# Kernel tuning notes

Hardware: AMD Instinct MI355X
Metric: run time of the kernel (lower is better)

The kernel has to match this reference:

```python
import jax, jax.numpy as jnp
import numpy as np

N = 50000          # num nodes
E = 600000         # num edges
F_IN = 128         # num_features
H = 128            # graph_hidden_dim
R = 2              # num_relations
L = 3              # n_layers_conv
BN_EPS = 1e-5
BN_BETA = 1e-4     # BatchNorm bias init per module code


def setup_inputs() -> dict:
    key = jax.random.key(0)
    ks = jax.random.split(key, 9)
    s_in = 1.0 / np.sqrt(F_IN)
    s_h = 1.0 / np.sqrt(H)
    return {
        "x": jax.random.normal(ks[0], (N, F_IN), jnp.float32),
        "edge_index": jax.random.randint(ks[1], (2, E), 0, N, jnp.int32),
        "edge_type": jax.random.randint(ks[2], (E,), 0, R, jnp.int32),
        "W0_rel": jax.random.normal(ks[3], (R, F_IN, H), jnp.float32) * s_in,
        "W0_root": jax.random.normal(ks[4], (F_IN, H), jnp.float32) * s_in,
        "b0": jnp.zeros((H,), jnp.float32),
        "Ws_rel": jax.random.normal(ks[5], (L, R, H, H), jnp.float32) * s_h,
        "Ws_root": jax.random.normal(ks[6], (L, H, H), jnp.float32) * s_h,
        "bs": jnp.zeros((L, H), jnp.float32),
    }


def batchnorm(x):
    # training-mode BatchNorm1d over nodes; weight=1, bias=1e-4 (per init)
    mu = jnp.mean(x, axis=0)
    var = jnp.mean((x - mu) ** 2, axis=0)  # biased var, as torch uses for norm
    return (x - mu) * jax.lax.rsqrt(var + BN_EPS) + BN_BETA


def rgcn_conv(x, src, dst, edge_type, W_rel, W_root, b):
    # PyG RGCNConv, aggr='mean': per-relation mean of x[src] at dst,
    # then per-relation linear, plus root transform and bias.
    seg = dst * R + edge_type  # combined (node, relation) segment id
    msgs = x[src]                                   # [E, d] gather
    sums = jax.ops.segment_sum(msgs, seg, num_segments=N * R)
    cnts = jax.ops.segment_sum(jnp.ones((src.shape[0],), x.dtype), seg,
                               num_segments=N * R)
    mean = sums.reshape(N, R, -1) / jnp.maximum(cnts, 1.0).reshape(N, R, 1)
    out = jnp.einsum('nrd,rdh->nh', mean, W_rel) + x @ W_root + b
    return out


def reference(x, edge_index, edge_type, W0_rel, W0_root, b0, Ws_rel, Ws_root, bs):
    src, dst = edge_index[0], edge_index[1]
    h = batchnorm(x)
    h = jax.nn.relu(rgcn_conv(h, src, dst, edge_type, W0_rel, W0_root, b0))
    for i in range(L):
        h_ = batchnorm(h)
        h_ = jax.nn.relu(rgcn_conv(h_, src, dst, edge_type,
                                   Ws_rel[i], Ws_root[i], bs[i]))
        h = h + h_  # conv_residual=True
    return h  # gconv_dropout == 0
```

## Files before the change

### kernel.cpp

```cpp
#include <hip/hip_runtime.h>
#include <hip/hip_bf16.h>

#define N_NODES 50000
#define N_EDGES 600000
#define F 128
#define R 2
#define NLAYER 4
#define NSEG (N_NODES * R)
#define SEGP (NSEG / 8)
#define NSCB 98
#define NB 384
#define STATS_STRIDE 2048
#define BN_EPS 1e-5f
#define BETA 1e-4f

typedef __hip_bfloat16 bf16;
typedef __attribute__((ext_vector_type(8))) short short8;
typedef __attribute__((ext_vector_type(4))) short short4x;
typedef __attribute__((ext_vector_type(4))) float floatx4;

__device__ __forceinline__ float b2f(short s) {
    union { unsigned u; float f; } c;
    c.u = ((unsigned)(unsigned short)s) << 16;
    return c.f;
}

__global__ void k_wt(const float* __restrict__ W0_rel, const float* __restrict__ W0_root,
                     const float* __restrict__ Ws_rel, const float* __restrict__ Ws_root,
                     bf16* __restrict__ Bt) {
    int idx = blockIdx.x * 256 + threadIdx.x;
    if (idx >= NLAYER * NB * F) return;
    int l = idx / (NB * F);
    int rem = idx % (NB * F);
    int j = rem / F, d = rem % F;
    float v;
    if (j < 256) {
        int r = j >> 7, c = j & 127;
        v = (l == 0) ? W0_rel[(r * F + d) * F + c]
                     : Ws_rel[((size_t)((l - 1) * R + r) * F + d) * F + c];
    } else {
        int c = j - 256;
        v = (l == 0) ? W0_root[d * F + c]
                     : Ws_root[((size_t)(l - 1) * F + d) * F + c];
    }
    Bt[idx] = __float2bfloat16(v);
}

__global__ void k_seg(const int* __restrict__ dst, const int* __restrict__ et,
                      int* __restrict__ seg) {
    int e = blockIdx.x * 256 + threadIdx.x;
    if (e < N_EDGES) seg[e] = dst[e] * R + et[e];
}

__global__ void k_count(const int* __restrict__ seg, int* __restrict__ cnt) {
    int g = blockIdx.x & 7;
    int lo = g * SEGP, hi = lo + SEGP;
    for (int e = (blockIdx.x >> 3) * 256 + threadIdx.x; e < N_EDGES; e += 65536) {
        int s = seg[e];
        if (s >= lo && s < hi) atomicAdd(&cnt[s], 1);
    }
}

__global__ void k_scan1(const int* __restrict__ cnt, int* __restrict__ off,
                        int* __restrict__ bsum) {
    int t = threadIdx.x;
    int g = blockIdx.x * 1024 + t;
    int v = (g < NSEG) ? cnt[g] : 0;
    int lane = t & 63;
    int wv = t >> 6;
    int x = v;
    for (int d = 1; d < 64; d <<= 1) {
        int y = __shfl_up(x, d, 64);
        if (lane >= d) x += y;
    }
    __shared__ int wtot[16];
    if (lane == 63) wtot[wv] = x;
    __syncthreads();
    if (t < 16) {
        int s = wtot[t];
        for (int d = 1; d < 16; d <<= 1) {
            int y = __shfl_up(s, d, 64);
            if (t >= d) s += y;
        }
        wtot[t] = s;
    }
    __syncthreads();
    int wpre = (wv == 0) ? 0 : wtot[wv - 1];
    int incl = x + wpre;
    if (g < NSEG) off[g] = incl - v;
    if (t == 1023) bsum[blockIdx.x] = incl;
}

__global__ void k_scan2(int* __restrict__ bsum) {
    __shared__ int s[128];
    int t = threadIdx.x;
    int v = (t < NSCB) ? bsum[t] : 0;
    s[t] = v;
    __syncthreads();
    for (int d = 1; d < 128; d <<= 1) {
        int y = (t >= d) ? s[t - d] : 0;
        __syncthreads();
        s[t] += y;
        __syncthreads();
    }
    if (t < NSCB) bsum[t] = s[t] - v;
}

__global__ void k_scan3(int* __restrict__ off, const int* __restrict__ bsum) {
    int g = blockIdx.x * 1024 + threadIdx.x;
    if (g < NSEG) off[g] += bsum[blockIdx.x];
}

__global__ void k_fill(const int* __restrict__ src, const int* __restrict__ seg,
                       const int* __restrict__ off,
                       int* __restrict__ fill, int* __restrict__ esrc) {
    int g = blockIdx.x & 7;
    int lo = g * SEGP, hi = lo + SEGP;
    for (int e = (blockIdx.x >> 3) * 256 + threadIdx.x; e < N_EDGES; e += 65536) {
        int s = seg[e];
        if (s >= lo && s < hi) {
            int idx = off[s] + atomicAdd(&fill[s], 1);
            esrc[idx] = src[e];
        }
    }
}

__global__ void k_bnstats(const float* __restrict__ h, float* __restrict__ gs) {
    int c = threadIdx.x & 127;
    int rl = threadIdx.x >> 7;
    float s = 0.f, q = 0.f;
    for (int r = blockIdx.x * 2 + rl; r < N_NODES; r += gridDim.x * 2) {
        float v = h[(size_t)r * F + c];
        s += v; q += v * v;
    }
    __shared__ float ls[256], lq[256];
    ls[threadIdx.x] = s; lq[threadIdx.x] = q;
    __syncthreads();
    if (rl == 0) {
        atomicAdd(&gs[c], ls[c] + ls[c + 128]);
        atomicAdd(&gs[128 + c], lq[c] + lq[c + 128]);
    }
}

__launch_bounds__(512)
__global__ void k_gemm(const float* __restrict__ h, const float* __restrict__ gs,
                       const bf16* __restrict__ Bt, const float* __restrict__ bias,
                       bf16* __restrict__ y, bf16* __restrict__ z) {
    __shared__ bf16 As[64 * 136];
    __shared__ bf16 Bs[128 * 136];
    int t = threadIdx.x;
    int m0 = blockIdx.x * 64;
    int c4 = (t & 31) * 4;
    float mu[4], rs[4];
    for (int c = 0; c < 4; c++) {
        float ssum = 0.f, qsum = 0.f;
        #pragma unroll
        for (int k = 0; k < 8; k++) {
            ssum += gs[k * 256 + c4 + c];
            qsum += gs[k * 256 + 128 + c4 + c];
        }
        float mm = ssum * (1.0f / N_NODES);
        float qq = qsum * (1.0f / N_NODES);
        mu[c] = mm;
        rs[c] = rsqrtf(qq - mm * mm + BN_EPS);
    }
    int r0 = t >> 5;
    for (int it = 0; it < 4; it++) {
        int row = r0 + it * 16;
        int m = m0 + row;
        float4 v = {0.f, 0.f, 0.f, 0.f};
        if (m < N_NODES) v = *(const float4*)(h + (size_t)m * F + c4);
        bf16 o[4];
        o[0] = __float2bfloat16((v.x - mu[0]) * rs[0] + BETA);
        o[1] = __float2bfloat16((v.y - mu[1]) * rs[1] + BETA);
        o[2] = __float2bfloat16((v.z - mu[2]) * rs[2] + BETA);
        o[3] = __float2bfloat16((v.w - mu[3]) * rs[3] + BETA);
        *(double*)(As + row * 136 + c4) = *(const double*)o;
    }
    __syncthreads();
    int w = t >> 6;
    int lane = t & 63;
    int msub = w & 3;
    int nh = w >> 2;
    int lm = lane & 15;
    int lq = lane >> 4;
    short8 a[4];
    for (int ki = 0; ki < 4; ki++)
        a[ki] = *(const short8*)(As + (msub * 16 + lm) * 136 + ki * 32 + lq * 8);
    int m = m0 + msub * 16 + lm;
    for (int ci = 0; ci < 3; ci++) {
        __syncthreads();
        {
            const bf16* bsrc = Bt + (size_t)ci * 128 * F;
            for (int rr = 0; rr < 4; rr++) {
                int idx = rr * 512 + t;
                int row = idx >> 4;
                int kc = idx & 15;
                short8 v = *(const short8*)(bsrc + row * F + kc * 8);
                *(short8*)(Bs + row * 136 + kc * 8) = v;
            }
        }
        __syncthreads();
        for (int tt = 0; tt < 4; tt++) {
            int nt = nh * 4 + tt;
            short8 b[4];
            for (int ki = 0; ki < 4; ki++)
                b[ki] = *(const short8*)(Bs + (nt * 16 + lm) * 136 + ki * 32 + lq * 8);
            floatx4 acc = {0.f, 0.f, 0.f, 0.f};
            for (int ki = 0; ki < 4; ki++)
                acc = __builtin_amdgcn_mfma_f32_16x16x32_bf16(b[ki], a[ki], acc, 0, 0, 0);
            int n0 = ci * 128 + nt * 16 + lq * 4;
            if (m < N_NODES) {
                if (ci < 2) {
                    union { bf16 o[4]; double d; } u;
                    u.o[0] = __float2bfloat16(acc[0]);
                    u.o[1] = __float2bfloat16(acc[1]);
                    u.o[2] = __float2bfloat16(acc[2]);
                    u.o[3] = __float2bfloat16(acc[3]);
                    *(double*)(y + (size_t)m * 256 + n0) = u.d;
                } else {
                    float4 bv = *(const float4*)(bias + (n0 - 256));
                    union { bf16 o[4]; double d; } u;
                    u.o[0] = __float2bfloat16(acc[0] + bv.x);
                    u.o[1] = __float2bfloat16(acc[1] + bv.y);
                    u.o[2] = __float2bfloat16(acc[2] + bv.z);
                    u.o[3] = __float2bfloat16(acc[3] + bv.w);
                    *(double*)(z + (size_t)m * F + (n0 - 256)) = u.d;
                }
            }
        }
    }
}

__global__ void k_aggregate(const bf16* __restrict__ y, const bf16* __restrict__ z,
                            const int* __restrict__ cnt, const int* __restrict__ off,
                            const int* __restrict__ esrc,
                            const float* __restrict__ hres, float* __restrict__ hout,
                            float* __restrict__ gs_next, int layer) {
    int wid = (blockIdx.x * 256 + threadIdx.x) >> 6;
    int lane = threadIdx.x & 63;
    int n = wid;
    int half = lane >> 5;
    int hl = lane & 31;
    int c4 = hl * 4;
    int2 cc = *(const int2*)(cnt + n * R);
    int o0 = off[n * R];
    int myc = half ? cc.y : cc.x;
    int myo = half ? (o0 + cc.x) : o0;
    float myinv = (myc > 0) ? 1.0f / (float)myc : 0.f;
    const bf16* yb = y + half * 128 + c4;
    float s0 = 0.f, s1 = 0.f, s2 = 0.f, s3 = 0.f;
    for (int i = 0; i < myc; i += 8) {
        int sn[8];
        #pragma unroll
        for (int k = 0; k < 8; k++) {
            int valid = (i + k < myc);
            sn[k] = esrc[valid ? (myo + i + k) : myo];
        }
        short4x p[8];
        #pragma unroll
        for (int k = 0; k < 8; k++)
            p[k] = *(const short4x*)(yb + (size_t)sn[k] * 256);
        #pragma unroll
        for (int k = 0; k < 8; k++) {
            float wk = (i + k < myc) ? myinv : 0.f;
            s0 = fmaf(b2f(p[k].x), wk, s0);
            s1 = fmaf(b2f(p[k].y), wk, s1);
            s2 = fmaf(b2f(p[k].z), wk, s2);
            s3 = fmaf(b2f(p[k].w), wk, s3);
        }
    }
    float t0 = __shfl_xor(s0, 32, 64);
    float t1 = __shfl_xor(s1, 32, 64);
    float t2 = __shfl_xor(s2, 32, 64);
    float t3 = __shfl_xor(s3, 32, 64);
    __shared__ float ls[4][128], lq[4][128];
    int wv = threadIdx.x >> 6;
    if (half == 0) {
        short4x zb = *(const short4x*)(z + (size_t)n * F + c4);
        float4 hp = {0.f, 0.f, 0.f, 0.f};
        if (layer > 0) hp = *(const float4*)(hres + (size_t)n * F + c4);
        float4 o4;
        o4.x = fmaxf(b2f(zb.x) + s0 + t0, 0.f) + hp.x;
        o4.y = fmaxf(b2f(zb.y) + s1 + t1, 0.f) + hp.y;
        o4.z = fmaxf(b2f(zb.z) + s2 + t2, 0.f) + hp.z;
        o4.w = fmaxf(b2f(zb.w) + s3 + t3, 0.f) + hp.w;
        *(float4*)(hout + (size_t)n * F + c4) = o4;
        if (gs_next) {
            ls[wv][c4 + 0] = o4.x; ls[wv][c4 + 1] = o4.y;
            ls[wv][c4 + 2] = o4.z; ls[wv][c4 + 3] = o4.w;
            lq[wv][c4 + 0] = o4.x * o4.x; lq[wv][c4 + 1] = o4.y * o4.y;
            lq[wv][c4 + 2] = o4.z * o4.z; lq[wv][c4 + 3] = o4.w * o4.w;
        }
    }
    if (gs_next) {
        __syncthreads();
        int t = threadIdx.x;
        float* gsc = gs_next + (blockIdx.x & 7) * 256;
        if (t < 128) {
            float S = (ls[0][t] + ls[1][t]) + (ls[2][t] + ls[3][t]);
            atomicAdd(&gsc[t], S);
        } else if (t < 256) {
            int c = t - 128;
            float Q = (lq[0][c] + lq[1][c]) + (lq[2][c] + lq[3][c]);
            atomicAdd(&gsc[128 + c], Q);
        }
    }
}

extern "C" void kernel_launch(void* const* d_in, const int* in_sizes, int n_in,
                              void* d_out, int out_size, void* d_ws, size_t ws_size,
                              hipStream_t stream) {
    const float* x       = (const float*)d_in[0];
    const int*   eidx    = (const int*)d_in[1];
    const int*   etype   = (const int*)d_in[2];
    const float* W0_rel  = (const float*)d_in[3];
    const float* W0_root = (const float*)d_in[4];
    const float* b0      = (const float*)d_in[5];
    const float* Ws_rel  = (const float*)d_in[6];
    const float* Ws_root = (const float*)d_in[7];
    const float* bs      = (const float*)d_in[8];
    const int* src = eidx;
    const int* dst = eidx + N_EDGES;

    char* w = (char*)d_ws;
    float* h   = (float*)w; w += (size_t)N_NODES * F * 4;
    bf16*  z   = (bf16*)w;  w += (size_t)N_NODES * F * 2;
    bf16*  y   = (bf16*)w;  w += (size_t)N_NODES * 256 * 2;
    bf16*  Bt  = (bf16*)w;  w += (size_t)NLAYER * NB * F * 2;
    int* cnt   = (int*)w;   w += (size_t)NSEG * 4;
    int* fill  = (int*)w;   w += (size_t)NSEG * 4;
    float* stats = (float*)w; w += (size_t)NLAYER * STATS_STRIDE * 4;
    int* off   = (int*)w;   w += (size_t)NSEG * 4;
    int* esrc  = (int*)w;   w += (size_t)N_EDGES * 4;
    int* segb  = (int*)w;   w += (size_t)N_EDGES * 4;
    int* bsum  = (int*)w;   w += 128 * 4;

    hipMemsetAsync(cnt, 0, (size_t)NSEG * 4 * 2 + (size_t)NLAYER * STATS_STRIDE * 4, stream);
    k_wt<<<(NLAYER * NB * F + 255) / 256, 256, 0, stream>>>(W0_rel, W0_root, Ws_rel, Ws_root, Bt);
    k_seg<<<(N_EDGES + 255) / 256, 256, 0, stream>>>(dst, etype, segb);
    k_count<<<2048, 256, 0, stream>>>(segb, cnt);
    k_scan1<<<NSCB, 1024, 0, stream>>>(cnt, off, bsum);
    k_scan2<<<1, 128, 0, stream>>>(bsum);
    k_scan3<<<NSCB, 1024, 0, stream>>>(off, bsum);
    k_fill<<<2048, 256, 0, stream>>>(src, segb, off, fill, esrc);
    k_bnstats<<<512, 256, 0, stream>>>(x, stats);

    for (int l = 0; l < NLAYER; l++) {
        const float* gsl = stats + (size_t)l * STATS_STRIDE;
        const float* bias = (l == 0) ? b0 : (bs + (size_t)(l - 1) * F);
        const float* hin = (l == 0) ? x : h;
        k_gemm<<<(N_NODES + 63) / 64, 512, 0, stream>>>(
            hin, gsl, Bt + (size_t)l * NB * F, bias, y, z);
        k_aggregate<<<(N_NODES * 64 + 255) / 256, 256, 0, stream>>>(
            y, z, cnt, off, esrc, h, (l == 3) ? (float*)d_out : h,
            (l < 3) ? (float*)(stats + (size_t)(l + 1) * STATS_STRIDE) : nullptr, l);
    }
}
```

Baseline: 449.9 us.

## Store inter-layer hidden state in bf16 and widen aggregate blocks to 512 threads

```diff
diff --git a/kernel.cpp b/kernel.cpp
--- a/kernel.cpp
+++ b/kernel.cpp
@@ -11,6 +11,7 @@
 #define NSCB 98
 #define NB 384
 #define STATS_STRIDE 2048
+#define AGGB 6250
 #define BN_EPS 1e-5f
 #define BETA 1e-4f
 
@@ -143,7 +144,8 @@
 }
 
 __launch_bounds__(512)
-__global__ void k_gemm(const float* __restrict__ h, const float* __restrict__ gs,
+__global__ void k_gemm(const void* __restrict__ hin, int in_bf16,
+                       const float* __restrict__ gs,
                        const bf16* __restrict__ Bt, const float* __restrict__ bias,
                        bf16* __restrict__ y, bf16* __restrict__ z) {
     __shared__ bf16 As[64 * 136];
@@ -168,13 +170,21 @@
     for (int it = 0; it < 4; it++) {
         int row = r0 + it * 16;
         int m = m0 + row;
-        float4 v = {0.f, 0.f, 0.f, 0.f};
-        if (m < N_NODES) v = *(const float4*)(h + (size_t)m * F + c4);
+        float f0 = 0.f, f1 = 0.f, f2 = 0.f, f3 = 0.f;
+        if (m < N_NODES) {
+            if (in_bf16) {
+                short4x v = *(const short4x*)((const bf16*)hin + (size_t)m * F + c4);
+                f0 = b2f(v.x); f1 = b2f(v.y); f2 = b2f(v.z); f3 = b2f(v.w);
+            } else {
+                float4 v = *(const float4*)((const float*)hin + (size_t)m * F + c4);
+                f0 = v.x; f1 = v.y; f2 = v.z; f3 = v.w;
+            }
+        }
         bf16 o[4];
-        o[0] = __float2bfloat16((v.x - mu[0]) * rs[0] + BETA);
-        o[1] = __float2bfloat16((v.y - mu[1]) * rs[1] + BETA);
-        o[2] = __float2bfloat16((v.z - mu[2]) * rs[2] + BETA);
-        o[3] = __float2bfloat16((v.w - mu[3]) * rs[3] + BETA);
+        o[0] = __float2bfloat16((f0 - mu[0]) * rs[0] + BETA);
+        o[1] = __float2bfloat16((f1 - mu[1]) * rs[1] + BETA);
+        o[2] = __float2bfloat16((f2 - mu[2]) * rs[2] + BETA);
+        o[3] = __float2bfloat16((f3 - mu[3]) * rs[3] + BETA);
         *(double*)(As + row * 136 + c4) = *(const double*)o;
     }
     __syncthreads();
@@ -232,12 +242,14 @@
     }
 }
 
+__launch_bounds__(512)
 __global__ void k_aggregate(const bf16* __restrict__ y, const bf16* __restrict__ z,
                             const int* __restrict__ cnt, const int* __restrict__ off,
                             const int* __restrict__ esrc,
-                            const float* __restrict__ hres, float* __restrict__ hout,
+                            const bf16* __restrict__ hres, bf16* __restrict__ hb_out,
+                            float* __restrict__ out_f32,
                             float* __restrict__ gs_next, int layer) {
-    int wid = (blockIdx.x * 256 + threadIdx.x) >> 6;
+    int wid = (blockIdx.x * 512 + threadIdx.x) >> 6;
     int lane = threadIdx.x & 63;
     int n = wid;
     int half = lane >> 5;
@@ -274,23 +286,41 @@
     float t1 = __shfl_xor(s1, 32, 64);
     float t2 = __shfl_xor(s2, 32, 64);
     float t3 = __shfl_xor(s3, 32, 64);
-    __shared__ float ls[4][128], lq[4][128];
+    __shared__ float ls[8][128], lq[8][128];
     int wv = threadIdx.x >> 6;
     if (half == 0) {
         short4x zb = *(const short4x*)(z + (size_t)n * F + c4);
         float4 hp = {0.f, 0.f, 0.f, 0.f};
-        if (layer > 0) hp = *(const float4*)(hres + (size_t)n * F + c4);
+        if (layer > 0) {
+            short4x hv = *(const short4x*)(hres + (size_t)n * F + c4);
+            hp.x = b2f(hv.x); hp.y = b2f(hv.y); hp.z = b2f(hv.z); hp.w = b2f(hv.w);
+        }
         float4 o4;
         o4.x = fmaxf(b2f(zb.x) + s0 + t0, 0.f) + hp.x;
         o4.y = fmaxf(b2f(zb.y) + s1 + t1, 0.f) + hp.y;
         o4.z = fmaxf(b2f(zb.z) + s2 + t2, 0.f) + hp.z;
         o4.w = fmaxf(b2f(zb.w) + s3 + t3, 0.f) + hp.w;
-        *(float4*)(hout + (size_t)n * F + c4) = o4;
-        if (gs_next) {
-            ls[wv][c4 + 0] = o4.x; ls[wv][c4 + 1] = o4.y;
-            ls[wv][c4 + 2] = o4.z; ls[wv][c4 + 3] = o4.w;
-            lq[wv][c4 + 0] = o4.x * o4.x; lq[wv][c4 + 1] = o4.y * o4.y;
-            lq[wv][c4 + 2] = o4.z * o4.z; lq[wv][c4 + 3] = o4.w * o4.w;
+        if (out_f32) {
+            *(float4*)(out_f32 + (size_t)n * F + c4) = o4;
+        } else {
+            short4x st;
+            st.x = *(short*)&(((bf16*)&st)[0]);
+            bf16 ob[4];
+            ob[0] = __float2bfloat16(o4.x);
+            ob[1] = __float2bfloat16(o4.y);
+            ob[2] = __float2bfloat16(o4.z);
+            ob[3] = __float2bfloat16(o4.w);
+            *(double*)(hb_out + (size_t)n * F + c4) = *(const double*)ob;
+            if (gs_next) {
+                float r0v = b2f(*(const short*)&ob[0]);
+                float r1v = b2f(*(const short*)&ob[1]);
+                float r2v = b2f(*(const short*)&ob[2]);
+                float r3v = b2f(*(const short*)&ob[3]);
+                ls[wv][c4 + 0] = r0v; ls[wv][c4 + 1] = r1v;
+                ls[wv][c4 + 2] = r2v; ls[wv][c4 + 3] = r3v;
+                lq[wv][c4 + 0] = r0v * r0v; lq[wv][c4 + 1] = r1v * r1v;
+                lq[wv][c4 + 2] = r2v * r2v; lq[wv][c4 + 3] = r3v * r3v;
+            }
         }
     }
     if (gs_next) {
@@ -298,11 +328,13 @@
         int t = threadIdx.x;
         float* gsc = gs_next + (blockIdx.x & 7) * 256;
         if (t < 128) {
-            float S = (ls[0][t] + ls[1][t]) + (ls[2][t] + ls[3][t]);
+            float S = ((ls[0][t] + ls[1][t]) + (ls[2][t] + ls[3][t]))
+                    + ((ls[4][t] + ls[5][t]) + (ls[6][t] + ls[7][t]));
             atomicAdd(&gsc[t], S);
         } else if (t < 256) {
             int c = t - 128;
-            float Q = (lq[0][c] + lq[1][c]) + (lq[2][c] + lq[3][c]);
+            float Q = ((lq[0][c] + lq[1][c]) + (lq[2][c] + lq[3][c]))
+                    + ((lq[4][c] + lq[5][c]) + (lq[6][c] + lq[7][c]));
             atomicAdd(&gsc[128 + c], Q);
         }
     }
@@ -324,7 +356,7 @@
     const int* dst = eidx + N_EDGES;
 
     char* w = (char*)d_ws;
-    float* h   = (float*)w; w += (size_t)N_NODES * F * 4;
+    bf16*  hb  = (bf16*)w;  w += (size_t)N_NODES * F * 2;
     bf16*  z   = (bf16*)w;  w += (size_t)N_NODES * F * 2;
     bf16*  y   = (bf16*)w;  w += (size_t)N_NODES * 256 * 2;
     bf16*  Bt  = (bf16*)w;  w += (size_t)NLAYER * NB * F * 2;
@@ -349,11 +381,12 @@
     for (int l = 0; l < NLAYER; l++) {
         const float* gsl = stats + (size_t)l * STATS_STRIDE;
         const float* bias = (l == 0) ? b0 : (bs + (size_t)(l - 1) * F);
-        const float* hin = (l == 0) ? x : h;
+        const void* hin = (l == 0) ? (const void*)x : (const void*)hb;
         k_gemm<<<(N_NODES + 63) / 64, 512, 0, stream>>>(
-            hin, gsl, Bt + (size_t)l * NB * F, bias, y, z);
-        k_aggregate<<<(N_NODES * 64 + 255) / 256, 256, 0, stream>>>(
-            y, z, cnt, off, esrc, h, (l == 3) ? (float*)d_out : h,
+            hin, (l > 0) ? 1 : 0, gsl, Bt + (size_t)l * NB * F, bias, y, z);
+        k_aggregate<<<AGGB, 512, 0, stream>>>(
+            y, z, cnt, off, esrc, hb, hb,
+            (l == 3) ? (float*)d_out : nullptr,
             (l < 3) ? (float*)(stats + (size_t)(l + 1) * STATS_STRIDE) : nullptr, l);
     }
 }
```

Result: faster. 423.7 us (-5.8%).
